# Performance work log

Hardware: AMD Instinct MI355X
Metric: run time of the kernel (lower is better)

## Reference

```python
import jax, jax.numpy as jnp
import numpy as np

INPUT_DIM = 512
NUM_CLASSES = 1000


def setup_inputs() -> dict:
    key = jax.random.key(0)
    kx, kw, kb = jax.random.split(key, 3)
    x = jax.random.normal(kx, (16384, INPUT_DIM), dtype=jnp.float32)
    # Stacked per-class Linear(input_dim, 2) params: W [C, 2, D], b [C, 2]
    lim = 1.0 / np.sqrt(INPUT_DIM)
    W = jax.random.uniform(kw, (NUM_CLASSES, 2, INPUT_DIM), dtype=jnp.float32, minval=-lim, maxval=lim)
    b = jax.random.uniform(kb, (NUM_CLASSES, 2), dtype=jnp.float32, minval=-lim, maxval=lim)
    return {"x": x, "W": W, "b": b}


def reference(x, W, b):
    # logits[b, c, t] = x[b, :] @ W[c, t, :] + b[c, t]
    logits = jnp.einsum("bd,ctd->bct", x, W) + b[None, :, :]  # [B, C, 2]
    # LogSoftmax over the 2 logits per class (torch dim=1 of the [B,2] slice)
    return jax.nn.log_softmax(logits, axis=-1)
```

## Files before the change

kernel.cpp:

```cpp
#include <hip/hip_runtime.h>
#include <cstdint>
#include <cstddef>

typedef unsigned short u16;
typedef unsigned int u32;
typedef __bf16 bf16x8 __attribute__((ext_vector_type(8)));
typedef float f32x4 __attribute__((ext_vector_type(4)));
typedef float f32x2 __attribute__((ext_vector_type(2)));

#define M_TOT 16384
#define C_TOT 1000
#define N_PAD 1024
#define K_TOT 512
#define OUT_STRIDE 2000
#define BM 128
#define BN 256
#define BK 32
#define KSTEPS (K_TOT / BK)
#define TILES_PER_BLOCK 2
#define NWG 256

__device__ __forceinline__ u16 f2bf(float f) {
  u32 u = __float_as_uint(f);
  u = (u + 0x7FFFu + ((u >> 16) & 1u)) >> 16;
  return (u16)u;
}

__global__ __launch_bounds__(256) void prep_kernel(const float* __restrict__ x,
                                                   const float* __restrict__ W,
                                                   const float* __restrict__ b,
                                                   u16* __restrict__ xb,
                                                   u16* __restrict__ wd,
                                                   float* __restrict__ bd) {
  if (blockIdx.x < 4096) {
    const int i = blockIdx.x * 256 + threadIdx.x;
    const float4* s = (const float4*)x;
    float4 a = s[2 * i], c = s[2 * i + 1];
    ushort4 r0, r1;
    r0.x = f2bf(a.x); r0.y = f2bf(a.y); r0.z = f2bf(a.z); r0.w = f2bf(a.w);
    r1.x = f2bf(c.x); r1.y = f2bf(c.y); r1.z = f2bf(c.z); r1.w = f2bf(c.w);
    ushort4* d = (ushort4*)xb;
    d[2 * i] = r0;
    d[2 * i + 1] = r1;
  } else {
    const int i = (blockIdx.x - 4096) * 256 + threadIdx.x;
    const int c = i >> 6;
    const int seg = i & 63;
    ushort4 r0 = {0, 0, 0, 0}, r1 = {0, 0, 0, 0};
    if (c < C_TOT) {
      const float4* w0 = (const float4*)(W + (size_t)(2 * c) * K_TOT) + seg * 2;
      const float4* w1 = (const float4*)(W + (size_t)(2 * c + 1) * K_TOT) + seg * 2;
      float4 a0 = w0[0], a1 = w0[1], c0 = w1[0], c1 = w1[1];
      r0.x = f2bf(a0.x - c0.x); r0.y = f2bf(a0.y - c0.y);
      r0.z = f2bf(a0.z - c0.z); r0.w = f2bf(a0.w - c0.w);
      r1.x = f2bf(a1.x - c1.x); r1.y = f2bf(a1.y - c1.y);
      r1.z = f2bf(a1.z - c1.z); r1.w = f2bf(a1.w - c1.w);
      if (seg == 0) bd[c] = b[2 * c] - b[2 * c + 1];
    } else if (seg == 0) {
      bd[c] = 0.0f;
    }
    ushort4* d = (ushort4*)(wd + (size_t)c * K_TOT);
    d[seg * 2] = r0;
    d[seg * 2 + 1] = r1;
  }
}

__device__ __forceinline__ void gload_lds(const u16* g, u16* l) {
  __builtin_amdgcn_global_load_lds((const __attribute__((address_space(1))) u32*)g,
                                   (__attribute__((address_space(3))) u32*)l, 16, 0, 0);
}

__global__ __launch_bounds__(512, 2) void gemm_ls_kernel(const u16* __restrict__ A,
                                                         const u16* __restrict__ B,
                                                         const float* __restrict__ bdiff,
                                                         float* __restrict__ out) {
  __shared__ u16 As[2][BM * BK];
  __shared__ u16 Bs[2][BN * BK];

  const int tid = threadIdx.x;
  const int lane = tid & 63;
  const int w = tid >> 6;
  const int wm = w >> 2;
  const int wn = w & 3;

  const int bid = blockIdx.x;
  const int wg = (bid & 7) * (NWG / 8) + (bid >> 3);
  const int m_base = (wg >> 2) * (BM * TILES_PER_BLOCK);
  const int n0 = (wg & 3) * BN;

  const int srow = tid >> 2;
  const int sg = tid & 3;
  const u16* gA = A + (size_t)(m_base + srow) * K_TOT + sg * 8;
  const u16* gB0 = B + (size_t)(n0 + srow) * K_TOT + sg * 8;
  const u16* gB1 = gB0 + (size_t)128 * K_TOT;

  const int loA = tid * 8;
  const int loB0 = tid * 8;
  const int loB1 = tid * 8 + 4096;

  const int ar = lane & 15;
  const int kq = (lane >> 4) * 16;

  gload_lds(gA, &As[0][loA]);
  gload_lds(gB0, &Bs[0][loB0]);
  gload_lds(gB1, &Bs[0][loB1]);

  int cur = 0;
#pragma unroll
  for (int t = 0; t < TILES_PER_BLOCK; ++t) {
    const u16* gAt = gA + (size_t)t * BM * K_TOT;
    f32x4 acc[4][4] = {};

    __syncthreads();

    for (int kt = 0; kt < KSTEPS; ++kt) {
      if (kt < KSTEPS - 1) {
        const int ko = (kt + 1) * BK;
        const int nb = cur ^ 1;
        gload_lds(gAt + ko, &As[nb][loA]);
        gload_lds(gB0 + ko, &Bs[nb][loB0]);
        gload_lds(gB1 + ko, &Bs[nb][loB1]);
      }

      bf16x8 af[4], bf[4];
#pragma unroll
      for (int mi = 0; mi < 4; ++mi) {
        const int row = wm * 64 + mi * 16 + ar;
        af[mi] = *(const bf16x8*)((const char*)&As[cur][0] + row * 64 + kq);
      }
#pragma unroll
      for (int ni = 0; ni < 4; ++ni) {
        const int row = wn * 64 + ni * 16 + ar;
        bf[ni] = *(const bf16x8*)((const char*)&Bs[cur][0] + row * 64 + kq);
      }
#pragma unroll
      for (int mi = 0; mi < 4; ++mi)
#pragma unroll
        for (int ni = 0; ni < 4; ++ni)
          acc[mi][ni] = __builtin_amdgcn_mfma_f32_16x16x32_bf16(af[mi], bf[ni], acc[mi][ni], 0, 0, 0);

      __syncthreads();
      cur ^= 1;
    }

    if (t + 1 < TILES_PER_BLOCK) {
      gload_lds(gAt + BM * K_TOT, &As[cur][loA]);
      gload_lds(gB0, &Bs[cur][loB0]);
      gload_lds(gB1, &Bs[cur][loB1]);
    }

    const int m0 = m_base + t * BM;
    const int rbase = m0 + wm * 64 + (lane >> 4) * 4;
    const bool full = (n0 + BN <= C_TOT);

#pragma unroll
    for (int ni = 0; ni < 4; ++ni) {
      const int n = n0 + wn * 64 + ni * 16 + ar;
      if (full || n < C_TOT) {
        const float bd_r = bdiff[n];
#pragma unroll
        for (int mi = 0; mi < 4; ++mi) {
#pragma unroll
          for (int j = 0; j < 4; ++j) {
            const float d = acc[mi][ni][j] + bd_r;
            const float o0 = fminf(d, 0.0f) - __logf(1.0f + __expf(-fabsf(d)));
            const int row = rbase + mi * 16 + j;
            f32x2 v;
            v.x = o0;
            v.y = o0 - d;
            *(f32x2*)(out + (size_t)row * OUT_STRIDE + 2 * n) = v;
          }
        }
      }
    }
  }
}

__global__ __launch_bounds__(256) void naive_kernel(const float* __restrict__ x,
                                                    const float* __restrict__ W,
                                                    const float* __restrict__ b,
                                                    float* __restrict__ out) {
  __shared__ float xs[K_TOT];
  const int row = blockIdx.x;
  for (int i = threadIdx.x; i < K_TOT; i += 256) xs[i] = x[(size_t)row * K_TOT + i];
  __syncthreads();
  for (int c = threadIdx.x; c < C_TOT; c += 256) {
    const float* w0 = W + (size_t)c * 1024;
    float l0 = b[c * 2], l1 = b[c * 2 + 1];
    for (int k = 0; k < K_TOT; ++k) {
      const float xv = xs[k];
      l0 += xv * w0[k];
      l1 += xv * w0[K_TOT + k];
    }
    const float d = l0 - l1;
    const float t = __logf(1.0f + __expf(-fabsf(d)));
    out[(size_t)row * OUT_STRIDE + c * 2]     = fminf(d, 0.0f) - t;
    out[(size_t)row * OUT_STRIDE + c * 2 + 1] = fminf(-d, 0.0f) - t;
  }
}

extern "C" void kernel_launch(void* const* d_in, const int* in_sizes, int n_in,
                              void* d_out, int out_size, void* d_ws, size_t ws_size,
                              hipStream_t stream) {
  const float* x = (const float*)d_in[0];
  const float* W = (const float*)d_in[1];
  const float* b = (const float*)d_in[2];
  float* out = (float*)d_out;

  const size_t nx = (size_t)M_TOT * K_TOT;
  const size_t nwd = (size_t)N_PAD * K_TOT;
  const size_t need = (nx + nwd) * sizeof(u16) + N_PAD * sizeof(float);

  if (ws_size < need) {
    naive_kernel<<<M_TOT, 256, 0, stream>>>(x, W, b, out);
    return;
  }

  u16* xb = (u16*)d_ws;
  u16* wd = xb + nx;
  float* bd = (float*)(wd + nwd);

  prep_kernel<<<4096 + 256, 256, 0, stream>>>(x, W, b, xb, wd, bd);
  gemm_ls_kernel<<<NWG, 512, 0, stream>>>(xb, wd, bd, out);
}
```

Baseline: 57.88 us.

## Retile GEMM to 128x128 with 4-stage LDS pipeline and XOR swizzle

Replaces the 128x256 tile (two M tiles per block, 512 threads, double buffer) with 128x128 tiles across 1024 blocks of 256 threads. Loads now go through a 4-deep LDS ring with explicit vmcnt waits, keeping three K-steps in flight and using a single barrier per step. The LDS layout is XOR-swizzled to cut bank conflicts on the fragment reads. The aim is more parallelism and better latency hiding. The cost is more blocks each re-reading the B operand, plus hand-tuned waitcnt logic that must match the load counts exactly.

Result: faster. 52.25 us (-9.7%).

```diff
diff --git a/kernel.cpp b/kernel.cpp
--- a/kernel.cpp
+++ b/kernel.cpp
@@ -14,11 +14,10 @@
 #define K_TOT 512
 #define OUT_STRIDE 2000
 #define BM 128
-#define BN 256
+#define BN 128
 #define BK 32
-#define KSTEPS (K_TOT / BK)
-#define TILES_PER_BLOCK 2
-#define NWG 256
+#define NT 16
+#define NWG 1024
 
 __device__ __forceinline__ u16 f2bf(float f) {
   u32 u = __float_as_uint(f);
@@ -70,110 +69,121 @@
                                    (__attribute__((address_space(3))) u32*)l, 16, 0, 0);
 }
 
-__global__ __launch_bounds__(512, 2) void gemm_ls_kernel(const u16* __restrict__ A,
+__device__ __forceinline__ void stage8k(const u16* __restrict__ gbase,
+                                        u16* lb, int tid) {
+#pragma unroll
+  for (int i = 0; i < 2; ++i) {
+    const int g = i * 256 + tid;
+    const int lrow = g >> 3;
+    const int u = (g & 7) ^ (lrow & 7);
+    const int r = lrow | ((u >> 2) << 6);
+    const int q = u & 3;
+    gload_lds(gbase + (size_t)r * K_TOT + q * 8, lb + (size_t)g * 8);
+  }
+}
+
+#define VMW(N) asm volatile("s_waitcnt vmcnt(" #N ")" ::: "memory")
+#define CFENCE asm volatile("" ::: "memory")
+
+__global__ __launch_bounds__(256, 2) void gemm_ls_kernel(const u16* __restrict__ A,
                                                          const u16* __restrict__ B,
                                                          const float* __restrict__ bdiff,
                                                          float* __restrict__ out) {
-  __shared__ u16 As[2][BM * BK];
-  __shared__ u16 Bs[2][BN * BK];
+  __shared__ u16 As[4][4096];
+  __shared__ u16 Bs[4][4096];
 
   const int tid = threadIdx.x;
   const int lane = tid & 63;
   const int w = tid >> 6;
-  const int wm = w >> 2;
-  const int wn = w & 3;
+  const int wm = w >> 1;
+  const int wn = w & 1;
 
   const int bid = blockIdx.x;
   const int wg = (bid & 7) * (NWG / 8) + (bid >> 3);
-  const int m_base = (wg >> 2) * (BM * TILES_PER_BLOCK);
-  const int n0 = (wg & 3) * BN;
-
-  const int srow = tid >> 2;
-  const int sg = tid & 3;
-  const u16* gA = A + (size_t)(m_base + srow) * K_TOT + sg * 8;
-  const u16* gB0 = B + (size_t)(n0 + srow) * K_TOT + sg * 8;
-  const u16* gB1 = gB0 + (size_t)128 * K_TOT;
-
-  const int loA = tid * 8;
-  const int loB0 = tid * 8;
-  const int loB1 = tid * 8 + 4096;
+  const int m0 = (wg >> 3) * BM;
+  const int n0 = (wg & 7) * BN;
+
+  const u16* gA = A + (size_t)m0 * K_TOT;
+  const u16* gB = B + (size_t)n0 * K_TOT;
 
   const int ar = lane & 15;
-  const int kq = (lane >> 4) * 16;
-
-  gload_lds(gA, &As[0][loA]);
-  gload_lds(gB0, &Bs[0][loB0]);
-  gload_lds(gB1, &Bs[0][loB1]);
-
-  int cur = 0;
-#pragma unroll
-  for (int t = 0; t < TILES_PER_BLOCK; ++t) {
-    const u16* gAt = gA + (size_t)t * BM * K_TOT;
-    f32x4 acc[4][4] = {};
-
-    __syncthreads();
-
-    for (int kt = 0; kt < KSTEPS; ++kt) {
-      if (kt < KSTEPS - 1) {
-        const int ko = (kt + 1) * BK;
-        const int nb = cur ^ 1;
-        gload_lds(gAt + ko, &As[nb][loA]);
-        gload_lds(gB0 + ko, &Bs[nb][loB0]);
-        gload_lds(gB1 + ko, &Bs[nb][loB1]);
-      }
-
-      bf16x8 af[4], bf[4];
+  const int kq4 = lane >> 4;
+  int offA[4], offB[4];
+#pragma unroll
+  for (int i = 0; i < 4; ++i) {
+    int r = wm * 64 + i * 16 + ar;
+    offA[i] = (r & 63) * 128 + (((((r >> 6) << 2) | kq4) ^ (r & 7)) << 4);
+    r = wn * 64 + i * 16 + ar;
+    offB[i] = (r & 63) * 128 + (((((r >> 6) << 2) | kq4) ^ (r & 7)) << 4);
+  }
+
+  f32x4 acc[4][4] = {};
+
+#define STAGEAB(t)                                   \
+  do {                                               \
+    const int _b = (t) & 3;                          \
+    stage8k(gA + (t) * BK, &As[_b][0], tid);         \
+    stage8k(gB + (t) * BK, &Bs[_b][0], tid);         \
+  } while (0)
+
+#define COMPUTE(cb)                                                         \
+  do {                                                                      \
+    bf16x8 af[4], bf[4];                                                    \
+    _Pragma("unroll") for (int i = 0; i < 4; ++i)                           \
+        af[i] = *(const bf16x8*)((const char*)&As[(cb)][0] + offA[i]);      \
+    _Pragma("unroll") for (int i = 0; i < 4; ++i)                           \
+        bf[i] = *(const bf16x8*)((const char*)&Bs[(cb)][0] + offB[i]);      \
+    _Pragma("unroll") for (int mi = 0; mi < 4; ++mi)                        \
+        _Pragma("unroll") for (int ni = 0; ni < 4; ++ni)                    \
+            acc[mi][ni] = __builtin_amdgcn_mfma_f32_16x16x32_bf16(          \
+                af[mi], bf[ni], acc[mi][ni], 0, 0, 0);                      \
+  } while (0)
+
+  STAGEAB(0);
+  STAGEAB(1);
+  STAGEAB(2);
+
+  for (int t = 0; t < 14; ++t) {
+    VMW(8);
+    __builtin_amdgcn_s_barrier();
+    CFENCE;
+    if (t < 13) STAGEAB(t + 3);
+    COMPUTE(t & 3);
+  }
+  VMW(4);
+  __builtin_amdgcn_s_barrier();
+  CFENCE;
+  COMPUTE(2);
+  VMW(0);
+  __builtin_amdgcn_s_barrier();
+  CFENCE;
+  COMPUTE(3);
+
+  const int rbase = m0 + wm * 64 + (lane >> 4) * 4;
+  const bool full = (n0 + BN <= C_TOT);
+
+#pragma unroll
+  for (int ni = 0; ni < 4; ++ni) {
+    const int n = n0 + wn * 64 + ni * 16 + ar;
+    if (full || n < C_TOT) {
+      const float bd_r = bdiff[n];
 #pragma unroll
       for (int mi = 0; mi < 4; ++mi) {
-        const int row = wm * 64 + mi * 16 + ar;
-        af[mi] = *(const bf16x8*)((const char*)&As[cur][0] + row * 64 + kq);
-      }
-#pragma unroll
-      for (int ni = 0; ni < 4; ++ni) {
-        const int row = wn * 64 + ni * 16 + ar;
-        bf[ni] = *(const bf16x8*)((const char*)&Bs[cur][0] + row * 64 + kq);
-      }
-#pragma unroll
-      for (int mi = 0; mi < 4; ++mi)
-#pragma unroll
-        for (int ni = 0; ni < 4; ++ni)
-          acc[mi][ni] = __builtin_amdgcn_mfma_f32_16x16x32_bf16(af[mi], bf[ni], acc[mi][ni], 0, 0, 0);
-
-      __syncthreads();
-      cur ^= 1;
-    }
-
-    if (t + 1 < TILES_PER_BLOCK) {
-      gload_lds(gAt + BM * K_TOT, &As[cur][loA]);
-      gload_lds(gB0, &Bs[cur][loB0]);
-      gload_lds(gB1, &Bs[cur][loB1]);
-    }
-
-    const int m0 = m_base + t * BM;
-    const int rbase = m0 + wm * 64 + (lane >> 4) * 4;
-    const bool full = (n0 + BN <= C_TOT);
-
-#pragma unroll
-    for (int ni = 0; ni < 4; ++ni) {
-      const int n = n0 + wn * 64 + ni * 16 + ar;
-      if (full || n < C_TOT) {
-        const float bd_r = bdiff[n];
-#pragma unroll
-        for (int mi = 0; mi < 4; ++mi) {
-#pragma unroll
-          for (int j = 0; j < 4; ++j) {
-            const float d = acc[mi][ni][j] + bd_r;
-            const float o0 = fminf(d, 0.0f) - __logf(1.0f + __expf(-fabsf(d)));
-            const int row = rbase + mi * 16 + j;
-            f32x2 v;
-            v.x = o0;
-            v.y = o0 - d;
-            *(f32x2*)(out + (size_t)row * OUT_STRIDE + 2 * n) = v;
-          }
+#pragma unroll
+        for (int j = 0; j < 4; ++j) {
+          const float d = acc[mi][ni][j] + bd_r;
+          const float o0 = fminf(d, 0.0f) - __logf(1.0f + __expf(-fabsf(d)));
+          const int row = rbase + mi * 16 + j;
+          f32x2 v;
+          v.x = o0;
+          v.y = o0 - d;
+          *(f32x2*)(out + (size_t)row * OUT_STRIDE + 2 * n) = v;
         }
       }
     }
   }
+#undef STAGEAB
+#undef COMPUTE
 }
 
 __global__ __launch_bounds__(256) void naive_kernel(const float* __restrict__ x,
@@ -221,5 +231,5 @@
   float* bd = (float*)(wd + nwd);
 
   prep_kernel<<<4096 + 256, 256, 0, stream>>>(x, W, b, xb, wd, bd);
-  gemm_ls_kernel<<<NWG, 512, 0, stream>>>(xb, wd, bd, out);
-}
+  gemm_ls_kernel<<<NWG, 256, 0, stream>>>(xb, wd, bd, out);
+}
```
